# Kernel optimization log

Measured on AMD Instinct MI355X. Metric: run time of the kernel, lower is better.

The kernel has to match this reference:

```python
import jax, jax.numpy as jnp
import numpy as np

B, T = 2, 512
E, NH, HD, V, P, L, KER, BLOCK = 768, 12, 64, 256, 4, 4, 16, 512
SCALE = HD ** -0.5


def _ln(x, g, b, eps=1e-5):
    m = jnp.mean(x, -1, keepdims=True)
    v = jnp.mean((x - m) ** 2, -1, keepdims=True)
    return (x - m) * jax.lax.rsqrt(v + eps) * g + b


def _rope_tables(n):
    inv = 1.0 / (10000.0 ** (jnp.arange(0, HD, 2, dtype=jnp.float32) / HD))
    f = jnp.arange(n, dtype=jnp.float32)[:, None] * inv[None, :]
    return jnp.cos(f), jnp.sin(f)


def _rope(x, cos, sin):
    # rotate over last two dims (positions, HD); split-half RoPE as in source
    h = x.shape[-1] // 2
    x1, x2 = x[..., :h], x[..., h:]
    return jnp.concatenate([x1 * cos - x2 * sin, x1 * sin + x2 * cos], axis=-1)


def _patch_attn(x, qkv_w, S):
    # x: [B,T,E]; sliding-window patch attention, step=1
    Bb, Tt, _ = x.shape
    q, k, v = jnp.split(x @ qkv_w, 3, axis=-1)
    heads = lambda t: t.reshape(Bb, Tt, NH, HD).transpose(0, 2, 1, 3)  # [B,NH,T,HD]
    q, k, v = heads(q), heads(k), heads(v)
    cos, sin = _rope_tables(Tt)
    q = _rope(q, cos, sin)
    k = _rope(k, cos, sin)
    # prefix: full causal attention over first S tokens
    sc = jnp.einsum('bnqh,bnkh->bnqk', q[:, :, :S], k[:, :, :S]) * SCALE
    mask = jnp.tril(jnp.ones((S, S), dtype=bool))
    sc = jnp.where(mask, sc, jnp.float32(-jnp.inf))
    out = jnp.einsum('bnqk,bnkh->bnqh', jax.nn.softmax(sc, axis=-1), v[:, :, :S])
    if Tt > S:
        # query t (t>=S) attends keys [t-S+1, t] (mask_sliding is all-ones for step=1)
        idx = jnp.arange(Tt - S)[:, None] + 1 + jnp.arange(S)[None, :]  # [T-S,S]
        kw = k[:, :, idx]  # [B,NH,T-S,S,HD]
        vw = v[:, :, idx]
        qs = q[:, :, S:]   # [B,NH,T-S,HD]
        sw = jnp.einsum('bnth,bntsh->bnts', qs, kw) * SCALE
        ow = jnp.einsum('bnts,bntsh->bnth', jax.nn.softmax(sw, axis=-1), vw)
        out = jnp.concatenate([out, ow], axis=2)
    return out.transpose(0, 2, 1, 3).reshape(Bb, Tt, NH * HD)


def _sa_block(x, ln0g, ln0b, ln1g, ln1b, qkv_w, proj_w, proj_b, w1, b1, w2, b2):
    # x: [B,T,P,V]; full (unmasked) attention over the P prediction slots
    Bb, Tt, Pp, _ = x.shape
    h = _ln(x, ln0g, ln0b)
    q, k, v = jnp.split(h @ qkv_w, 3, axis=-1)
    heads = lambda t: t.reshape(Bb, Tt, Pp, NH, HD).transpose(0, 1, 3, 2, 4)  # [B,T,NH,P,HD]
    q, k, v = heads(q), heads(k), heads(v)
    cos, sin = _rope_tables(Pp)
    q = _rope(q, cos, sin)
    k = _rope(k, cos, sin)
    sc = jnp.einsum('btnph,btnqh->btnpq', q, k) * SCALE
    o = jnp.einsum('btnpq,btnqh->btnph', jax.nn.softmax(sc, axis=-1), v)
    o = o.transpose(0, 1, 3, 2, 4).reshape(Bb, Tt, Pp, NH * HD)
    x = x + (o @ proj_w + proj_b)
    h2 = _ln(x, ln1g, ln1b)
    ff = jax.nn.gelu(h2 @ w1 + b1, approximate=False) @ w2 + b2
    return x + ff


def _forward(tokens, emb, blk_ln0_g, blk_ln0_b, blk_ln1_g, blk_ln1_b, blk_qkv_w,
             blk_ff_w1, blk_ff_b1, blk_ff_w2, blk_ff_b2, fin_ln_g, fin_ln_b,
             head_w, head_b, sa_ln0_g, sa_ln0_b, sa_ln1_g, sa_ln1_b, sa_qkv_w,
             sa_proj_w, sa_proj_b, sa_ff_w1, sa_ff_b1, sa_ff_w2, sa_ff_b2):
    x0 = emb[tokens]  # [B,T,E]
    x = x0
    for i in range(L):
        S = min(KER * 2 ** i, BLOCK)
        h = _ln(x, blk_ln0_g[i], blk_ln0_b[i])
        x = x + _patch_attn(h, blk_qkv_w[i], S)
        h2 = _ln(x, blk_ln1_g[i], blk_ln1_b[i])
        x = x + (jax.nn.gelu(h2 @ blk_ff_w1[i] + blk_ff_b1[i], approximate=False)
                 @ blk_ff_w2[i] + blk_ff_b2[i])
    x = x0 + x  # Golu: x = token_embedding(x); x = x + blocks(x)
    x = _ln(x, fin_ln_g, fin_ln_b)
    logits = (x @ head_w + head_b).reshape(B, T, P, V)
    logits = _sa_block(logits, sa_ln0_g, sa_ln0_b, sa_ln1_g, sa_ln1_b, sa_qkv_w,
                       sa_proj_w, sa_proj_b, sa_ff_w1, sa_ff_b1, sa_ff_w2, sa_ff_b2)
    return logits[:, :, 0, :]  # [B,T,V] (y is None path)


def setup_inputs() -> dict:
    key = jax.random.key(0)
    ks = jax.random.split(key, 12)
    w = lambda k, sh: jax.random.normal(k, sh, dtype=jnp.float32) * 0.02
    return {
        'tokens': jax.random.randint(ks[0], (B, T), 0, V),
        'emb': w(ks[1], (V, E)),
        'blk_ln0_g': jnp.ones((L, E), jnp.float32),
        'blk_ln0_b': jnp.zeros((L, E), jnp.float32),
        'blk_ln1_g': jnp.ones((L, E), jnp.float32),
        'blk_ln1_b': jnp.zeros((L, E), jnp.float32),
        'blk_qkv_w': w(ks[2], (L, E, 3 * E)),
        'blk_ff_w1': w(ks[3], (L, E, 4 * E)),
        'blk_ff_b1': jnp.zeros((L, 4 * E), jnp.float32),
        'blk_ff_w2': w(ks[4], (L, 4 * E, E)),
        'blk_ff_b2': jnp.zeros((L, E), jnp.float32),
        'fin_ln_g': jnp.ones((E,), jnp.float32),
        'fin_ln_b': jnp.zeros((E,), jnp.float32),
        'head_w': w(ks[5], (E, V * P)),
        'head_b': jnp.zeros((V * P,), jnp.float32),
        'sa_ln0_g': jnp.ones((V,), jnp.float32),
        'sa_ln0_b': jnp.zeros((V,), jnp.float32),
        'sa_ln1_g': jnp.ones((V,), jnp.float32),
        'sa_ln1_b': jnp.zeros((V,), jnp.float32),
        'sa_qkv_w': w(ks[6], (V, 3 * E)),
        'sa_proj_w': w(ks[7], (E, V)),
        'sa_proj_b': jnp.zeros((V,), jnp.float32),
        'sa_ff_w1': w(ks[8], (V, 4 * V)),
        'sa_ff_b1': jnp.zeros((4 * V,), jnp.float32),
        'sa_ff_w2': w(ks[9], (4 * V, V)),
        'sa_ff_b2': jnp.zeros((V,), jnp.float32),
    }


def reference(tokens, emb, blk_ln0_g, blk_ln0_b, blk_ln1_g, blk_ln1_b, blk_qkv_w,
              blk_ff_w1, blk_ff_b1, blk_ff_w2, blk_ff_b2, fin_ln_g, fin_ln_b,
              head_w, head_b, sa_ln0_g, sa_ln0_b, sa_ln1_g, sa_ln1_b, sa_qkv_w,
              sa_proj_w, sa_proj_b, sa_ff_w1, sa_ff_b1, sa_ff_w2, sa_ff_b2):
    return _forward(tokens, emb, blk_ln0_g, blk_ln0_b, blk_ln1_g, blk_ln1_b,
                    blk_qkv_w, blk_ff_w1, blk_ff_b1, blk_ff_w2, blk_ff_b2,
                    fin_ln_g, fin_ln_b, head_w, head_b, sa_ln0_g, sa_ln0_b,
                    sa_ln1_g, sa_ln1_b, sa_qkv_w, sa_proj_w, sa_proj_b,
                    sa_ff_w1, sa_ff_b1, sa_ff_w2, sa_ff_b2)
```

## Files before the change

kernel.cpp:

```cpp
#include <hip/hip_runtime.h>
#include <hip/hip_bf16.h>
#include <cstdint>
#include <cstddef>

#define BB    2
#define TSEQ  512
#define EDIM  768
#define NHEAD 12
#define HDIM  64
#define VDIM  256
#define PDIM  4
#define NROW  (BB*TSEQ)
#define NROW2 (BB*TSEQ*PDIM)

typedef __attribute__((ext_vector_type(8))) short short8;
typedef __attribute__((ext_vector_type(4))) float floatx4;

__device__ __forceinline__ float gelu_f(float v){
    return 0.5f * v * (1.0f + erff(v * 0.70710678118654752f));
}

__device__ __forceinline__ float b2f(short s){
    unsigned u = ((unsigned)(unsigned short)s) << 16;
    float f; __builtin_memcpy(&f, &u, 4); return f;
}

__device__ __forceinline__ void gload16(const void* g, void* l){
    __builtin_amdgcn_global_load_lds((const __attribute__((address_space(1))) void*)g,
                                     (__attribute__((address_space(3))) void*)l, 16, 0, 0);
}

struct WD { const float* in; __hip_bfloat16* out; int K; int N; int ntiles; };

__global__ __launch_bounds__(256) void wconv_multi(WD d0, WD d1, WD d2, WD d3, WD d4)
{
    int id = blockIdx.x;
    WD w = d0;
    if(id >= w.ntiles){ id -= w.ntiles; w = d1;
        if(id >= w.ntiles){ id -= w.ntiles; w = d2;
            if(id >= w.ntiles){ id -= w.ntiles; w = d3;
                if(id >= w.ntiles){ id -= w.ntiles; w = d4; } } } }
    if(!w.in) return;
    const int tx = w.N / 32;
    const int n0 = (id % tx) * 32, k0 = (id / tx) * 32;
    __shared__ float t[32][33];
    const int c = threadIdx.x & 31, r0 = threadIdx.x >> 5;
    #pragma unroll
    for(int r = r0; r < 32; r += 8)
        t[r][c] = w.in[(size_t)(k0 + r) * w.N + n0 + c];
    __syncthreads();
    #pragma unroll
    for(int r = r0; r < 32; r += 8)
        w.out[(size_t)(n0 + r) * w.K + k0 + c] = __float2bfloat16(t[c][r]);
}

template<int ACT, int RESID, int OUTBF16, int ROPESA>
__global__ __launch_bounds__(256) void gemm128(
    const short* __restrict__ A, const short* __restrict__ Bt,
    const float* __restrict__ bias, const float* __restrict__ resid,
    void* __restrict__ Cout, const float* __restrict__ rc, const float* __restrict__ rs,
    int M, int N, int K)
{
    alignas(16) __shared__ short As[128*32];
    alignas(16) __shared__ short Bs[128*32];
    const int tid  = threadIdx.x;
    const int lane = tid & 63;
    const int wave = tid >> 6;
    const int bm = blockIdx.y * 128, bn = blockIdx.x * 128;
    const int wm = (wave >> 1) * 64, wn = (wave & 1) * 64;
    const int quad = lane >> 4, l16 = lane & 15;

    floatx4 acc[4][4];
    #pragma unroll
    for(int i = 0; i < 4; i++)
        #pragma unroll
        for(int j = 0; j < 4; j++)
            acc[i][j] = floatx4{0.f, 0.f, 0.f, 0.f};

    const int r  = tid >> 2;
    const int c8 = (tid & 3) * 8;
    const int ldsoff = (tid & 192) * 16;

    for(int k0 = 0; k0 < K; k0 += 32){
        gload16(A  + (size_t)(bm + r     ) * K + k0 + c8, (char*)As + ldsoff);
        gload16(A  + (size_t)(bm + r + 64) * K + k0 + c8, (char*)As + 4096 + ldsoff);
        gload16(Bt + (size_t)(bn + r     ) * K + k0 + c8, (char*)Bs + ldsoff);
        gload16(Bt + (size_t)(bn + r + 64) * K + k0 + c8, (char*)Bs + 4096 + ldsoff);
        __syncthreads();
        short8 af[4], bfr[4];
        #pragma unroll
        for(int i = 0; i < 4; i++){
            af[i]  = *(const short8*)&As[(wm + i*16 + l16)*32 + quad*8];
            bfr[i] = *(const short8*)&Bs[(wn + i*16 + l16)*32 + quad*8];
        }
        #pragma unroll
        for(int i = 0; i < 4; i++)
            #pragma unroll
            for(int j = 0; j < 4; j++)
                acc[i][j] = __builtin_amdgcn_mfma_f32_16x16x32_bf16(af[i], bfr[j], acc[i][j], 0, 0, 0);
        __syncthreads();
    }

    float* Cf = (float*)Cout;
    __hip_bfloat16* Cb = (__hip_bfloat16*)Cout;

    if(ROPESA){
        const int hb = bn + wn;
        const int region = hb / 768;
        #pragma unroll
        for(int i = 0; i < 4; i++){
            #pragma unroll
            for(int rr = 0; rr < 4; rr++){
                int row = bm + wm + i*16 + quad*4 + rr;
                float a0 = acc[i][0][rr], a1 = acc[i][1][rr];
                float a2 = acc[i][2][rr], a3 = acc[i][3][rr];
                size_t rowb = (size_t)row * N + hb;
                if(region == 2){
                    Cb[rowb + l16]      = __float2bfloat16(a0);
                    Cb[rowb + 16 + l16] = __float2bfloat16(a1);
                    Cb[rowb + 32 + l16] = __float2bfloat16(a2);
                    Cb[rowb + 48 + l16] = __float2bfloat16(a3);
                }else{
                    int p = row & 3;
                    float c0 = rc[p*32 + l16],      s0 = rs[p*32 + l16];
                    float c1 = rc[p*32 + 16 + l16], s1 = rs[p*32 + 16 + l16];
                    Cb[rowb + l16]      = __float2bfloat16(a0*c0 - a2*s0);
                    Cb[rowb + 16 + l16] = __float2bfloat16(a1*c1 - a3*s1);
                    Cb[rowb + 32 + l16] = __float2bfloat16(a0*s0 + a2*c0);
                    Cb[rowb + 48 + l16] = __float2bfloat16(a1*s1 + a3*c1);
                }
            }
        }
        return;
    }

    #pragma unroll
    for(int i = 0; i < 4; i++){
        int row0 = bm + wm + i*16 + quad*4;
        #pragma unroll
        for(int j = 0; j < 4; j++){
            int col = bn + wn + j*16 + l16;
            float bv = bias ? bias[col] : 0.f;
            #pragma unroll
            for(int rr = 0; rr < 4; rr++){
                float v = acc[i][j][rr] + bv;
                if(ACT) v = gelu_f(v);
                if(RESID) v += resid[(size_t)(row0 + rr) * N + col];
                if(OUTBF16) Cb[(size_t)(row0 + rr) * N + col] = __float2bfloat16(v);
                else        Cf[(size_t)(row0 + rr) * N + col] = v;
            }
        }
    }
}

template<int EPI>
__global__ __launch_bounds__(256) void gemm64x128(
    const short* __restrict__ A, const short* __restrict__ Bt,
    const float* __restrict__ bias, __hip_bfloat16* __restrict__ Cout,
    __hip_bfloat16* __restrict__ qrb, __hip_bfloat16* __restrict__ krb,
    __hip_bfloat16* __restrict__ vvb,
    const float* __restrict__ rc, const float* __restrict__ rs,
    int M, int N, int K)
{
    alignas(16) __shared__ short As[64*32];
    alignas(16) __shared__ short Bs[128*32];
    const int tid  = threadIdx.x;
    const int lane = tid & 63;
    const int wave = tid >> 6;
    const int bm = blockIdx.y * 64, bn = blockIdx.x * 128;
    const int wm = (wave >> 1) * 32, wn = (wave & 1) * 64;
    const int quad = lane >> 4, l16 = lane & 15;

    floatx4 acc[2][4];
    #pragma unroll
    for(int i = 0; i < 2; i++)
        #pragma unroll
        for(int j = 0; j < 4; j++)
            acc[i][j] = floatx4{0.f, 0.f, 0.f, 0.f};

    const int r  = tid >> 2;
    const int c8 = (tid & 3) * 8;
    const int ldsoff = (tid & 192) * 16;

    for(int k0 = 0; k0 < K; k0 += 32){
        gload16(A  + (size_t)(bm + r     ) * K + k0 + c8, (char*)As + ldsoff);
        gload16(Bt + (size_t)(bn + r     ) * K + k0 + c8, (char*)Bs + ldsoff);
        gload16(Bt + (size_t)(bn + r + 64) * K + k0 + c8, (char*)Bs + 4096 + ldsoff);
        __syncthreads();
        short8 af[2], bfr[4];
        #pragma unroll
        for(int i = 0; i < 2; i++)
            af[i]  = *(const short8*)&As[(wm + i*16 + l16)*32 + quad*8];
        #pragma unroll
        for(int j = 0; j < 4; j++)
            bfr[j] = *(const short8*)&Bs[(wn + j*16 + l16)*32 + quad*8];
        #pragma unroll
        for(int i = 0; i < 2; i++)
            #pragma unroll
            for(int j = 0; j < 4; j++)
                acc[i][j] = __builtin_amdgcn_mfma_f32_16x16x32_bf16(af[i], bfr[j], acc[i][j], 0, 0, 0);
        __syncthreads();
    }

    if(EPI == 2){
        const int hb = bn + wn;
        const int region = hb / 768;
        const int h = (hb % 768) >> 6;
        #pragma unroll
        for(int i = 0; i < 2; i++){
            #pragma unroll
            for(int rr = 0; rr < 4; rr++){
                int row = bm + wm + i*16 + quad*4 + rr;
                int t = row & (TSEQ-1), b = row >> 9;
                float a0 = acc[i][0][rr], a1 = acc[i][1][rr];
                float a2 = acc[i][2][rr], a3 = acc[i][3][rr];
                size_t dbase = ((size_t)(b*NHEAD + h)*TSEQ + t)*HDIM;
                if(region == 2){
                    vvb[dbase + l16]      = __float2bfloat16(a0);
                    vvb[dbase + 16 + l16] = __float2bfloat16(a1);
                    vvb[dbase + 32 + l16] = __float2bfloat16(a2);
                    vvb[dbase + 48 + l16] = __float2bfloat16(a3);
                }else{
                    float c0 = rc[t*32 + l16],      s0 = rs[t*32 + l16];
                    float c1 = rc[t*32 + 16 + l16], s1 = rs[t*32 + 16 + l16];
                    __hip_bfloat16* dst = (region == 0) ? qrb : krb;
                    dst[dbase + l16]      = __float2bfloat16(a0*c0 - a2*s0);
                    dst[dbase + 16 + l16] = __float2bfloat16(a1*c1 - a3*s1);
                    dst[dbase + 32 + l16] = __float2bfloat16(a0*s0 + a2*c0);
                    dst[dbase + 48 + l16] = __float2bfloat16(a1*s1 + a3*c1);
                }
            }
        }
        return;
    }

    #pragma unroll
    for(int i = 0; i < 2; i++){
        int row0 = bm + wm + i*16 + quad*4;
        #pragma unroll
        for(int j = 0; j < 4; j++){
            int col = bn + wn + j*16 + l16;
            float bv = bias ? bias[col] : 0.f;
            #pragma unroll
            for(int rr = 0; rr < 4; rr++){
                float v = acc[i][j][rr] + bv;
                if(EPI == 1) v = gelu_f(v);
                Cout[(size_t)(row0 + rr) * N + col] = __float2bfloat16(v);
            }
        }
    }
}

template<int ACT, int RESID, int OUTBF16>
__global__ __launch_bounds__(256) void gemm64t(
    const short* __restrict__ A, const short* __restrict__ Bt,
    const float* __restrict__ bias, const float* __restrict__ resid,
    void* __restrict__ Cout, int M, int N, int K)
{
    alignas(16) __shared__ short As[64*32];
    alignas(16) __shared__ short Bs[64*32];
    const int tid  = threadIdx.x;
    const int lane = tid & 63;
    const int wave = tid >> 6;
    const int bm = blockIdx.y * 64, bn = blockIdx.x * 64;
    const int wm = (wave >> 1) * 32, wn = (wave & 1) * 32;
    const int quad = lane >> 4, l16 = lane & 15;

    floatx4 acc[2][2];
    #pragma unroll
    for(int i = 0; i < 2; i++)
        #pragma unroll
        for(int j = 0; j < 2; j++)
            acc[i][j] = floatx4{0.f, 0.f, 0.f, 0.f};

    const int r  = tid >> 2;
    const int c8 = (tid & 3) * 8;
    const int ldsoff = (tid & 192) * 16;

    for(int k0 = 0; k0 < K; k0 += 32){
        gload16(A  + (size_t)(bm + r) * K + k0 + c8, (char*)As + ldsoff);
        gload16(Bt + (size_t)(bn + r) * K + k0 + c8, (char*)Bs + ldsoff);
        __syncthreads();
        short8 af[2], bfr[2];
        #pragma unroll
        for(int i = 0; i < 2; i++){
            af[i]  = *(const short8*)&As[(wm + i*16 + l16)*32 + quad*8];
            bfr[i] = *(const short8*)&Bs[(wn + i*16 + l16)*32 + quad*8];
        }
        #pragma unroll
        for(int i = 0; i < 2; i++)
            #pragma unroll
            for(int j = 0; j < 2; j++)
                acc[i][j] = __builtin_amdgcn_mfma_f32_16x16x32_bf16(af[i], bfr[j], acc[i][j], 0, 0, 0);
        __syncthreads();
    }

    float* Cf = (float*)Cout;
    __hip_bfloat16* Cb = (__hip_bfloat16*)Cout;
    #pragma unroll
    for(int i = 0; i < 2; i++){
        int row0 = bm + wm + i*16 + quad*4;
        #pragma unroll
        for(int j = 0; j < 2; j++){
            int col = bn + wn + j*16 + l16;
            float bv = bias ? bias[col] : 0.f;
            #pragma unroll
            for(int rr = 0; rr < 4; rr++){
                float v = acc[i][j][rr] + bv;
                if(ACT) v = gelu_f(v);
                if(RESID) v += resid[(size_t)(row0 + rr) * N + col];
                if(OUTBF16) Cb[(size_t)(row0 + rr) * N + col] = __float2bfloat16(v);
                else        Cf[(size_t)(row0 + rr) * N + col] = v;
            }
        }
    }
}

__global__ __launch_bounds__(256) void ln_kernel(
    const float* __restrict__ in, const float* __restrict__ in2,
    const float* __restrict__ g, const float* __restrict__ bta,
    __hip_bfloat16* __restrict__ out, int D)
{
    const int row = blockIdx.x;
    const float* xr  = in + (size_t)row * D;
    const float* x2r = in2 ? in2 + (size_t)row * D : nullptr;
    const int tid = threadIdx.x;
    const int nper = D / 256;
    float vals[3];
    float sum = 0.f, sq = 0.f;
    for(int i = 0; i < nper; i++){
        int d = tid + i*256;
        float v = xr[d];
        if(x2r) v += x2r[d];
        vals[i] = v; sum += v; sq += v*v;
    }
    #pragma unroll
    for(int off = 32; off > 0; off >>= 1){
        sum += __shfl_xor(sum, off, 64);
        sq  += __shfl_xor(sq,  off, 64);
    }
    __shared__ float ssum[4], ssq[4];
    __shared__ float smean, srstd;
    int wid = tid >> 6;
    if((tid & 63) == 0){ ssum[wid] = sum; ssq[wid] = sq; }
    __syncthreads();
    if(tid == 0){
        float S = 0.f, Q = 0.f;
        for(int w = 0; w < 4; w++){ S += ssum[w]; Q += ssq[w]; }
        float m = S / D;
        float var = Q / D - m*m;
        smean = m;
        srstd = rsqrtf(fmaxf(var, 0.f) + 1e-5f);
    }
    __syncthreads();
    float m = smean, rs2 = srstd;
    for(int i = 0; i < nper; i++){
        int d = tid + i*256;
        out[(size_t)row*D + d] = __float2bfloat16((vals[i] - m) * rs2 * g[d] + bta[d]);
    }
}

__global__ __launch_bounds__(192) void embed_kernel(
    const int* __restrict__ tokens, const float* __restrict__ emb,
    float* __restrict__ x0, float* __restrict__ x)
{
    const int row = blockIdx.x;
    const int tok = tokens[row];
    const float4* src = (const float4*)(emb + (size_t)tok * EDIM);
    float4* d0 = (float4*)(x0 + (size_t)row * EDIM);
    float4* d1 = (float4*)(x  + (size_t)row * EDIM);
    for(int i = threadIdx.x; i < EDIM/4; i += blockDim.x){
        float4 v = src[i]; d0[i] = v; d1[i] = v;
    }
}

__global__ __launch_bounds__(256) void rope_kernel(float* __restrict__ rc, float* __restrict__ rs)
{
    int i = blockIdx.x * 256 + threadIdx.x;
    int pos = i >> 5, d = i & 31;
    float inv = powf(10000.0f, -(float)(2*d) / 64.0f);
    float f = (float)pos * inv;
    rc[i] = cosf(f);
    rs[i] = sinf(f);
}

template<int S>
__global__ __launch_bounds__(256) void patch_attn2(
    const __hip_bfloat16* __restrict__ qr, const __hip_bfloat16* __restrict__ kr,
    const __hip_bfloat16* __restrict__ vv, float* __restrict__ x)
{
    constexpr int W = S + 3;
    alignas(16) __shared__ short Ks[W*64];
    alignas(16) __shared__ short Vs[W*64];
    __shared__ float qlds[4*64];
    __shared__ float pb[4*128];

    const int t0 = blockIdx.x * 4;
    const int h = blockIdx.y, b = blockIdx.z;
    const int tid = threadIdx.x;
    const int wv = tid >> 6, lane = tid & 63;
    const size_t headbase = ((size_t)(b*NHEAD + h)) * TSEQ;

    const int c = tid & 7;
    for(int r = tid >> 3; r < W; r += 32){
        int g = t0 - S + 1 + r;
        int gc = g < 0 ? 0 : g;
        int sc = (c ^ (r & 7)) * 8;
        *(short8*)&Ks[r*64 + sc] = *(const short8*)((const short*)kr + (headbase + gc)*64 + c*8);
        *(short8*)&Vs[r*64 + sc] = *(const short8*)((const short*)vv + (headbase + gc)*64 + c*8);
    }
    qlds[wv*64 + lane] = __bfloat162float(qr[(headbase + t0 + wv)*64 + lane]);
    __syncthreads();

    const int t = t0 + wv;
    const int r0 = (S >= 64) ? (wv + lane) : ((lane < S) ? (wv + lane) : 0);
    const int r1 = wv + lane + 64;
    float a0 = 0.f, a1 = 0.f;
    #pragma unroll
    for(int ch = 0; ch < 8; ch++){
        float4 qa = *(const float4*)&qlds[wv*64 + ch*8];
        float4 qb = *(const float4*)&qlds[wv*64 + ch*8 + 4];
        short8 k0 = *(const short8*)&Ks[r0*64 + ((ch ^ (r0 & 7))*8)];
        a0 += qa.x*b2f(k0[0]) + qa.y*b2f(k0[1]) + qa.z*b2f(k0[2]) + qa.w*b2f(k0[3])
            + qb.x*b2f(k0[4]) + qb.y*b2f(k0[5]) + qb.z*b2f(k0[6]) + qb.w*b2f(k0[7]);
        if(S == 128){
            short8 k1 = *(const short8*)&Ks[r1*64 + ((ch ^ (r1 & 7))*8)];
            a1 += qa.x*b2f(k1[0]) + qa.y*b2f(k1[1]) + qa.z*b2f(k1[2]) + qa.w*b2f(k1[3])
                + qb.x*b2f(k1[4]) + qb.y*b2f(k1[5]) + qb.z*b2f(k1[6]) + qb.w*b2f(k1[7]);
        }
    }
    const int key0 = t - S + 1 + lane;
    const bool v0 = (lane < S) && (key0 >= 0);
    const bool v1 = (S == 128) && (key0 + 64 >= 0);
    float s0 = v0 ? a0 * 0.125f : -1e30f;
    float s1 = v1 ? a1 * 0.125f : -1e30f;
    float mx = fmaxf(s0, s1);
    #pragma unroll
    for(int off = 32; off > 0; off >>= 1) mx = fmaxf(mx, __shfl_xor(mx, off, 64));
    float p0 = v0 ? expf(s0 - mx) : 0.f;
    float p1 = v1 ? expf(s1 - mx) : 0.f;
    float sm = p0 + p1;
    #pragma unroll
    for(int off = 32; off > 0; off >>= 1) sm += __shfl_xor(sm, off, 64);
    const float inv = 1.f / sm;
    pb[wv*128 + lane] = p0 * inv;
    if(S == 128) pb[wv*128 + lane + 64] = p1 * inv;
    __syncthreads();

    const int d = lane;
    const int coff = d >> 3, dlo = d & 7;
    float o = 0.f;
    #pragma unroll 8
    for(int j = 0; j < S; j++){
        int r = wv + j;
        float p = pb[wv*128 + j];
        o += p * b2f(Vs[r*64 + ((coff ^ (r & 7))*8) + dlo]);
    }
    x[((size_t)(b*TSEQ) + t) * EDIM + h*HDIM + d] += o;
}

__global__ __launch_bounds__(256) void sa_attn(
    const __hip_bfloat16* __restrict__ qkv2, __hip_bfloat16* __restrict__ o)
{
    const int t = blockIdx.x, h = blockIdx.y, b = blockIdx.z;
    const int p = threadIdx.x >> 6, lane = threadIdx.x & 63;
    const int row0 = (b*TSEQ + t) * PDIM;
    const short* base = (const short*)qkv2 + (size_t)row0 * (3*EDIM);
    const int d = lane;
    float q = b2f(base[(size_t)p*(3*EDIM) + h*HDIM + d]);
    float sc[4];
    #pragma unroll
    for(int j = 0; j < 4; j++){
        float kj = b2f(base[(size_t)j*(3*EDIM) + EDIM + h*HDIM + d]);
        float v = q * kj;
        #pragma unroll
        for(int off = 32; off > 0; off >>= 1) v += __shfl_xor(v, off, 64);
        sc[j] = v * 0.125f;
    }
    float m = fmaxf(fmaxf(sc[0], sc[1]), fmaxf(sc[2], sc[3]));
    float e0 = expf(sc[0]-m), e1 = expf(sc[1]-m), e2 = expf(sc[2]-m), e3 = expf(sc[3]-m);
    float idn = 1.f / (e0 + e1 + e2 + e3);
    float ov = (e0 * b2f(base[0*(3*EDIM) + 2*EDIM + h*HDIM + d])
              + e1 * b2f(base[1*(3*EDIM) + 2*EDIM + h*HDIM + d])
              + e2 * b2f(base[2*(3*EDIM) + 2*EDIM + h*HDIM + d])
              + e3 * b2f(base[3*(3*EDIM) + 2*EDIM + h*HDIM + d])) * idn;
    o[(size_t)(row0 + p) * EDIM + h*HDIM + d] = __float2bfloat16(ov);
}

__global__ __launch_bounds__(256) void outcopy(const float* __restrict__ x2, float* __restrict__ out)
{
    int i = blockIdx.x * 256 + threadIdx.x;
    int row = i >> 8, col = i & 255;
    out[i] = x2[(size_t)row * PDIM * VDIM + col];
}

extern "C" void kernel_launch(void* const* d_in, const int* in_sizes, int n_in,
                              void* d_out, int out_size, void* d_ws, size_t ws_size,
                              hipStream_t stream)
{
    const int*   tokens    = (const int*)  d_in[0];
    const float* emb       = (const float*)d_in[1];
    const float* bl0g      = (const float*)d_in[2];
    const float* bl0b      = (const float*)d_in[3];
    const float* bl1g      = (const float*)d_in[4];
    const float* bl1b      = (const float*)d_in[5];
    const float* qkv_w     = (const float*)d_in[6];
    const float* ff_w1     = (const float*)d_in[7];
    const float* ff_b1     = (const float*)d_in[8];
    const float* ff_w2     = (const float*)d_in[9];
    const float* ff_b2     = (const float*)d_in[10];
    const float* fin_g     = (const float*)d_in[11];
    const float* fin_b     = (const float*)d_in[12];
    const float* head_w    = (const float*)d_in[13];
    const float* head_b    = (const float*)d_in[14];
    const float* sa_ln0_g  = (const float*)d_in[15];
    const float* sa_ln0_b  = (const float*)d_in[16];
    const float* sa_ln1_g  = (const float*)d_in[17];
    const float* sa_ln1_b  = (const float*)d_in[18];
    const float* sa_qkv_w  = (const float*)d_in[19];
    const float* sa_proj_w = (const float*)d_in[20];
    const float* sa_proj_b = (const float*)d_in[21];
    const float* sa_ff_w1  = (const float*)d_in[22];
    const float* sa_ff_b1  = (const float*)d_in[23];
    const float* sa_ff_w2  = (const float*)d_in[24];
    const float* sa_ff_b2  = (const float*)d_in[25];
    float* out = (float*)d_out;

    char* base = (char*)d_ws;
    float* logits           = (float*)(base);
    float* ropec            = (float*)(base + 4194304);
    float* ropes            = (float*)(base + 4259840);
    __hip_bfloat16* wqkvT   = (__hip_bfloat16*)(base + 4325376);
    __hip_bfloat16* wff1T   = (__hip_bfloat16*)(base + 7864320);
    __hip_bfloat16* wff2T   = (__hip_bfloat16*)(base + 12582912);
    __hip_bfloat16* wheadT  = (__hip_bfloat16*)(base + 17301504);
    __hip_bfloat16* wsaqkvT = (__hip_bfloat16*)(base + 18874368);
    __hip_bfloat16* wsaprojT= (__hip_bfloat16*)(base + 20054016);
    __hip_bfloat16* wsaff1T = (__hip_bfloat16*)(base + 20447232);
    __hip_bfloat16* wsaff2T = (__hip_bfloat16*)(base + 20971520);
    char* U = base + 21495808;
    float* x0           = (float*)(U);
    float* x            = (float*)(U + 3145728);
    __hip_bfloat16* h   = (__hip_bfloat16*)(U + 6291456);
    __hip_bfloat16* ff1 = (__hip_bfloat16*)(U + 12582912);
    __hip_bfloat16* qrb = (__hip_bfloat16*)(U + 18874368);
    __hip_bfloat16* krb = (__hip_bfloat16*)(U + 20447232);
    __hip_bfloat16* vvb = (__hip_bfloat16*)(U + 22020096);
    __hip_bfloat16* h2    = (__hip_bfloat16*)(U);
    __hip_bfloat16* qkv2  = (__hip_bfloat16*)(U + 2097152);
    __hip_bfloat16* sa_o  = (__hip_bfloat16*)(U + 20971520);
    __hip_bfloat16* sa_f1 = (__hip_bfloat16*)(U + 27262976);

    embed_kernel<<<NROW, 192, 0, stream>>>(tokens, emb, x0, x);
    rope_kernel<<<64, 256, 0, stream>>>(ropec, ropes);
    {
        WD dh  = { head_w,    wheadT,   768,  1024, (1024/32)*( 768/32) };
        WD dq  = { sa_qkv_w,  wsaqkvT,  256,  2304, (2304/32)*( 256/32) };
        WD dp  = { sa_proj_w, wsaprojT, 768,   256, ( 256/32)*( 768/32) };
        WD df1 = { sa_ff_w1,  wsaff1T,  256,  1024, (1024/32)*( 256/32) };
        WD df2 = { sa_ff_w2,  wsaff2T, 1024,   256, ( 256/32)*(1024/32) };
        wconv_multi<<<768+576+192+256+256, 256, 0, stream>>>(dh, dq, dp, df1, df2);
    }

    for(int i = 0; i < 4; i++){
        {
            WD dq  = { qkv_w + (size_t)i*EDIM*3*EDIM, wqkvT, 768, 2304, (2304/32)*(768/32) };
            WD df1 = { ff_w1 + (size_t)i*EDIM*4*EDIM, wff1T, 768, 3072, (3072/32)*(768/32) };
            WD df2 = { ff_w2 + (size_t)i*4*EDIM*EDIM, wff2T, 3072, 768, ( 768/32)*(3072/32)};
            WD dn  = { nullptr, nullptr, 0, 0, 0 };
            wconv_multi<<<1728+2304+2304, 256, 0, stream>>>(dq, df1, df2, dn, dn);
        }
        ln_kernel<<<NROW, 256, 0, stream>>>(x, nullptr, bl0g + i*EDIM, bl0b + i*EDIM, h, EDIM);
        gemm64x128<2><<<dim3(18, 16), 256, 0, stream>>>(
            (const short*)h, (const short*)wqkvT, nullptr, nullptr,
            qrb, krb, vvb, ropec, ropes, NROW, 3*EDIM, EDIM);
        dim3 agrid(TSEQ/4, NHEAD, BB);
        if(i == 0)      patch_attn2<16><<<agrid, 256, 0, stream>>>(qrb, krb, vvb, x);
        else if(i == 1) patch_attn2<32><<<agrid, 256, 0, stream>>>(qrb, krb, vvb, x);
        else if(i == 2) patch_attn2<64><<<agrid, 256, 0, stream>>>(qrb, krb, vvb, x);
        else            patch_attn2<128><<<agrid, 256, 0, stream>>>(qrb, krb, vvb, x);
        ln_kernel<<<NROW, 256, 0, stream>>>(x, nullptr, bl1g + i*EDIM, bl1b + i*EDIM, h, EDIM);
        gemm64x128<1><<<dim3(24, 16), 256, 0, stream>>>(
            (const short*)h, (const short*)wff1T, ff_b1 + (size_t)i*4*EDIM, ff1,
            nullptr, nullptr, nullptr, nullptr, nullptr, NROW, 4*EDIM, EDIM);
        gemm64t<0,1,0><<<dim3(12, 16), 256, 0, stream>>>(
            (const short*)ff1, (const short*)wff2T, ff_b2 + (size_t)i*EDIM, x, x, NROW, EDIM, 4*EDIM);
    }

    ln_kernel<<<NROW, 256, 0, stream>>>(x, x0, fin_g, fin_b, h, EDIM);
    gemm64t<0,0,0><<<dim3(16, 16), 256, 0, stream>>>(
        (const short*)h, (const short*)wheadT, head_b, nullptr, logits, NROW, PDIM*VDIM, EDIM);

    ln_kernel<<<NROW2, 256, 0, stream>>>(logits, nullptr, sa_ln0_g, sa_ln0_b, h2, VDIM);
    gemm128<0,0,1,1><<<dim3(18, 32), 256, 0, stream>>>(
        (const short*)h2, (const short*)wsaqkvT, nullptr, nullptr, qkv2,
        ropec, ropes, NROW2, 3*EDIM, VDIM);
    sa_attn<<<dim3(TSEQ, NHEAD, BB), 256, 0, stream>>>(qkv2, sa_o);
    gemm64t<0,1,0><<<dim3(4, 64), 256, 0, stream>>>(
        (const short*)sa_o, (const short*)wsaprojT, sa_proj_b, logits, logits, NROW2, VDIM, EDIM);
    ln_kernel<<<NROW2, 256, 0, stream>>>(logits, nullptr, sa_ln1_g, sa_ln1_b, h2, VDIM);
    gemm128<1,0,1,0><<<dim3(8, 32), 256, 0, stream>>>(
        (const short*)h2, (const short*)wsaff1T, sa_ff_b1, nullptr, sa_f1,
        nullptr, nullptr, NROW2, 4*VDIM, VDIM);
    gemm64t<0,1,0><<<dim3(4, 64), 256, 0, stream>>>(
        (const short*)sa_f1, (const short*)wsaff2T, sa_ff_b2, logits, logits, NROW2, VDIM, 4*VDIM);

    outcopy<<<(out_size + 255)/256, 256, 0, stream>>>(logits, out);
}
```

Measured before the change: 736.5 us.

## Convert all weights in one launch and fuse output copy into final GEMM

Replaces the per-layer weight transpose/convert launches with a single wconv_all kernel that converts all 17 weight matrices up front into separate per-layer bf16 buffers. It uses 64x64 tiles with float4 loads and short4 stores. The final SA FF2 GEMM now also writes every fourth row (slot 0) directly to the output, which removes the separate outcopy kernel. This cuts launch count and serialization between layers, at the cost of more workspace and a larger struct argument for the kernel.

```diff
diff --git a/kernel.cpp b/kernel.cpp
--- a/kernel.cpp
+++ b/kernel.cpp
@@ -19,39 +19,48 @@
 __device__ __forceinline__ float gelu_f(float v){
     return 0.5f * v * (1.0f + erff(v * 0.70710678118654752f));
 }
-
 __device__ __forceinline__ float b2f(short s){
     unsigned u = ((unsigned)(unsigned short)s) << 16;
     float f; __builtin_memcpy(&f, &u, 4); return f;
 }
-
+__device__ __forceinline__ short f2bs(float v){
+    __hip_bfloat16 h = __float2bfloat16(v);
+    short s; __builtin_memcpy(&s, &h, 2); return s;
+}
 __device__ __forceinline__ void gload16(const void* g, void* l){
     __builtin_amdgcn_global_load_lds((const __attribute__((address_space(1))) void*)g,
                                      (__attribute__((address_space(3))) void*)l, 16, 0, 0);
 }
 
-struct WD { const float* in; __hip_bfloat16* out; int K; int N; int ntiles; };
-
-__global__ __launch_bounds__(256) void wconv_multi(WD d0, WD d1, WD d2, WD d3, WD d4)
+struct WD2 { const float* in; __hip_bfloat16* out; int K; int N; int nt; };
+struct WDs { WD2 d[17]; };
+
+__global__ __launch_bounds__(256) void wconv_all(WDs a)
 {
     int id = blockIdx.x;
-    WD w = d0;
-    if(id >= w.ntiles){ id -= w.ntiles; w = d1;
-        if(id >= w.ntiles){ id -= w.ntiles; w = d2;
-            if(id >= w.ntiles){ id -= w.ntiles; w = d3;
-                if(id >= w.ntiles){ id -= w.ntiles; w = d4; } } } }
-    if(!w.in) return;
-    const int tx = w.N / 32;
-    const int n0 = (id % tx) * 32, k0 = (id / tx) * 32;
-    __shared__ float t[32][33];
-    const int c = threadIdx.x & 31, r0 = threadIdx.x >> 5;
-    #pragma unroll
-    for(int r = r0; r < 32; r += 8)
-        t[r][c] = w.in[(size_t)(k0 + r) * w.N + n0 + c];
+    int i = 0;
+    while(i < 16 && id >= a.d[i].nt){ id -= a.d[i].nt; i++; }
+    WD2 w = a.d[i];
+    const int tx = w.N / 64;
+    const int n0 = (id % tx) * 64, k0 = (id / tx) * 64;
+    __shared__ float t[64][65];
+    const int cg = (threadIdx.x & 15) * 4;
+    const int rr = threadIdx.x >> 4;
+    #pragma unroll
+    for(int it = 0; it < 4; it++){
+        int r = rr + it*16;
+        float4 v = *(const float4*)(w.in + (size_t)(k0 + r) * w.N + n0 + cg);
+        t[r][cg+0] = v.x; t[r][cg+1] = v.y; t[r][cg+2] = v.z; t[r][cg+3] = v.w;
+    }
     __syncthreads();
     #pragma unroll
-    for(int r = r0; r < 32; r += 8)
-        w.out[(size_t)(n0 + r) * w.K + k0 + c] = __float2bfloat16(t[c][r]);
+    for(int it = 0; it < 4; it++){
+        int n = rr + it*16;
+        short4 o;
+        o.x = f2bs(t[cg+0][n]); o.y = f2bs(t[cg+1][n]);
+        o.z = f2bs(t[cg+2][n]); o.w = f2bs(t[cg+3][n]);
+        *(short4*)((short*)w.out + (size_t)(n0 + n) * w.K + k0 + cg) = o;
+    }
 }
 
 template<int ACT, int RESID, int OUTBF16, int ROPESA>
@@ -251,11 +260,11 @@
     }
 }
 
-template<int ACT, int RESID, int OUTBF16>
+template<int RESID, int OUTC>
 __global__ __launch_bounds__(256) void gemm64t(
     const short* __restrict__ A, const short* __restrict__ Bt,
     const float* __restrict__ bias, const float* __restrict__ resid,
-    void* __restrict__ Cout, int M, int N, int K)
+    float* __restrict__ Cf, float* __restrict__ outp, int M, int N, int K)
 {
     alignas(16) __shared__ short As[64*32];
     alignas(16) __shared__ short Bs[64*32];
@@ -295,8 +304,6 @@
         __syncthreads();
     }
 
-    float* Cf = (float*)Cout;
-    __hip_bfloat16* Cb = (__hip_bfloat16*)Cout;
     #pragma unroll
     for(int i = 0; i < 2; i++){
         int row0 = bm + wm + i*16 + quad*4;
@@ -306,11 +313,12 @@
             float bv = bias ? bias[col] : 0.f;
             #pragma unroll
             for(int rr = 0; rr < 4; rr++){
+                int row = row0 + rr;
                 float v = acc[i][j][rr] + bv;
-                if(ACT) v = gelu_f(v);
-                if(RESID) v += resid[(size_t)(row0 + rr) * N + col];
-                if(OUTBF16) Cb[(size_t)(row0 + rr) * N + col] = __float2bfloat16(v);
-                else        Cf[(size_t)(row0 + rr) * N + col] = v;
+                if(RESID) v += resid[(size_t)row * N + col];
+                Cf[(size_t)row * N + col] = v;
+                if(OUTC && (row & 3) == 0)
+                    outp[(size_t)(row >> 2) * N + col] = v;
             }
         }
     }
@@ -485,13 +493,6 @@
               + e2 * b2f(base[2*(3*EDIM) + 2*EDIM + h*HDIM + d])
               + e3 * b2f(base[3*(3*EDIM) + 2*EDIM + h*HDIM + d])) * idn;
     o[(size_t)(row0 + p) * EDIM + h*HDIM + d] = __float2bfloat16(ov);
-}
-
-__global__ __launch_bounds__(256) void outcopy(const float* __restrict__ x2, float* __restrict__ out)
-{
-    int i = blockIdx.x * 256 + threadIdx.x;
-    int row = i >> 8, col = i & 255;
-    out[i] = x2[(size_t)row * PDIM * VDIM + col];
 }
 
 extern "C" void kernel_launch(void* const* d_in, const int* in_sizes, int n_in,
@@ -526,26 +527,28 @@
     const float* sa_ff_b2  = (const float*)d_in[25];
     float* out = (float*)d_out;
 
-    char* base = (char*)d_ws;
-    float* logits           = (float*)(base);
-    float* ropec            = (float*)(base + 4194304);
-    float* ropes            = (float*)(base + 4259840);
-    __hip_bfloat16* wqkvT   = (__hip_bfloat16*)(base + 4325376);
-    __hip_bfloat16* wff1T   = (__hip_bfloat16*)(base + 7864320);
-    __hip_bfloat16* wff2T   = (__hip_bfloat16*)(base + 12582912);
-    __hip_bfloat16* wheadT  = (__hip_bfloat16*)(base + 17301504);
-    __hip_bfloat16* wsaqkvT = (__hip_bfloat16*)(base + 18874368);
-    __hip_bfloat16* wsaprojT= (__hip_bfloat16*)(base + 20054016);
-    __hip_bfloat16* wsaff1T = (__hip_bfloat16*)(base + 20447232);
-    __hip_bfloat16* wsaff2T = (__hip_bfloat16*)(base + 20971520);
-    char* U = base + 21495808;
+    char* p = (char*)d_ws;
+    auto alloc = [&](size_t bytes){ char* q = p; p += (bytes + 255) & ~(size_t)255; return q; };
+
+    float* logits = (float*)alloc((size_t)NROW2*VDIM*4);
+    float* ropec  = (float*)alloc(512*32*4);
+    float* ropes  = (float*)alloc(512*32*4);
+    __hip_bfloat16* wqkvT[4]; for(int i=0;i<4;i++) wqkvT[i] = (__hip_bfloat16*)alloc((size_t)768*2304*2);
+    __hip_bfloat16* wff1T[4]; for(int i=0;i<4;i++) wff1T[i] = (__hip_bfloat16*)alloc((size_t)768*3072*2);
+    __hip_bfloat16* wff2T[4]; for(int i=0;i<4;i++) wff2T[i] = (__hip_bfloat16*)alloc((size_t)3072*768*2);
+    __hip_bfloat16* wheadT   = (__hip_bfloat16*)alloc((size_t)768*1024*2);
+    __hip_bfloat16* wsaqkvT  = (__hip_bfloat16*)alloc((size_t)256*2304*2);
+    __hip_bfloat16* wsaprojT = (__hip_bfloat16*)alloc((size_t)768*256*2);
+    __hip_bfloat16* wsaff1T  = (__hip_bfloat16*)alloc((size_t)256*1024*2);
+    __hip_bfloat16* wsaff2T  = (__hip_bfloat16*)alloc((size_t)1024*256*2);
+    char* U = p;
     float* x0           = (float*)(U);
     float* x            = (float*)(U + 3145728);
     __hip_bfloat16* h   = (__hip_bfloat16*)(U + 6291456);
-    __hip_bfloat16* ff1 = (__hip_bfloat16*)(U + 12582912);
-    __hip_bfloat16* qrb = (__hip_bfloat16*)(U + 18874368);
-    __hip_bfloat16* krb = (__hip_bfloat16*)(U + 20447232);
-    __hip_bfloat16* vvb = (__hip_bfloat16*)(U + 22020096);
+    __hip_bfloat16* ff1 = (__hip_bfloat16*)(U + 7864320);
+    __hip_bfloat16* qrb = (__hip_bfloat16*)(U + 14155776);
+    __hip_bfloat16* krb = (__hip_bfloat16*)(U + 15728640);
+    __hip_bfloat16* vvb = (__hip_bfloat16*)(U + 17301504);
     __hip_bfloat16* h2    = (__hip_bfloat16*)(U);
     __hip_bfloat16* qkv2  = (__hip_bfloat16*)(U + 2097152);
     __hip_bfloat16* sa_o  = (__hip_bfloat16*)(U + 20971520);
@@ -554,25 +557,28 @@
     embed_kernel<<<NROW, 192, 0, stream>>>(tokens, emb, x0, x);
     rope_kernel<<<64, 256, 0, stream>>>(ropec, ropes);
     {
-        WD dh  = { head_w,    wheadT,   768,  1024, (1024/32)*( 768/32) };
-        WD dq  = { sa_qkv_w,  wsaqkvT,  256,  2304, (2304/32)*( 256/32) };
-        WD dp  = { sa_proj_w, wsaprojT, 768,   256, ( 256/32)*( 768/32) };
-        WD df1 = { sa_ff_w1,  wsaff1T,  256,  1024, (1024/32)*( 256/32) };
-        WD df2 = { sa_ff_w2,  wsaff2T, 1024,   256, ( 256/32)*(1024/32) };
-        wconv_multi<<<768+576+192+256+256, 256, 0, stream>>>(dh, dq, dp, df1, df2);
+        WDs wds; int tot = 0, n = 0;
+        auto add = [&](const float* in, __hip_bfloat16* o2, int K, int N){
+            wds.d[n++] = WD2{in, o2, K, N, (N/64)*(K/64)};
+            tot += (N/64)*(K/64);
+        };
+        for(int i=0;i<4;i++){
+            add(qkv_w + (size_t)i*768*2304, wqkvT[i], 768, 2304);
+            add(ff_w1 + (size_t)i*768*3072, wff1T[i], 768, 3072);
+            add(ff_w2 + (size_t)i*3072*768, wff2T[i], 3072, 768);
+        }
+        add(head_w,    wheadT,   768, 1024);
+        add(sa_qkv_w,  wsaqkvT,  256, 2304);
+        add(sa_proj_w, wsaprojT, 768, 256);
+        add(sa_ff_w1,  wsaff1T,  256, 1024);
+        add(sa_ff_w2,  wsaff2T, 1024, 256);
+        wconv_all<<<tot, 256, 0, stream>>>(wds);
     }
 
     for(int i = 0; i < 4; i++){
-        {
-            WD dq  = { qkv_w + (size_t)i*EDIM*3*EDIM, wqkvT, 768, 2304, (2304/32)*(768/32) };
-            WD df1 = { ff_w1 + (size_t)i*EDIM*4*EDIM, wff1T, 768, 3072, (3072/32)*(768/32) };
-            WD df2 = { ff_w2 + (size_t)i*4*EDIM*EDIM, wff2T, 3072, 768, ( 768/32)*(3072/32)};
-            WD dn  = { nullptr, nullptr, 0, 0, 0 };
-            wconv_multi<<<1728+2304+2304, 256, 0, stream>>>(dq, df1, df2, dn, dn);
-        }
         ln_kernel<<<NROW, 256, 0, stream>>>(x, nullptr, bl0g + i*EDIM, bl0b + i*EDIM, h, EDIM);
         gemm64x128<2><<<dim3(18, 16), 256, 0, stream>>>(
-            (const short*)h, (const short*)wqkvT, nullptr, nullptr,
+            (const short*)h, (const short*)wqkvT[i], nullptr, nullptr,
             qrb, krb, vvb, ropec, ropes, NROW, 3*EDIM, EDIM);
         dim3 agrid(TSEQ/4, NHEAD, BB);
         if(i == 0)      patch_attn2<16><<<agrid, 256, 0, stream>>>(qrb, krb, vvb, x);
@@ -581,29 +587,31 @@
         else            patch_attn2<128><<<agrid, 256, 0, stream>>>(qrb, krb, vvb, x);
         ln_kernel<<<NROW, 256, 0, stream>>>(x, nullptr, bl1g + i*EDIM, bl1b + i*EDIM, h, EDIM);
         gemm64x128<1><<<dim3(24, 16), 256, 0, stream>>>(
-            (const short*)h, (const short*)wff1T, ff_b1 + (size_t)i*4*EDIM, ff1,
+            (const short*)h, (const short*)wff1T[i], ff_b1 + (size_t)i*4*EDIM, ff1,
             nullptr, nullptr, nullptr, nullptr, nullptr, NROW, 4*EDIM, EDIM);
-        gemm64t<0,1,0><<<dim3(12, 16), 256, 0, stream>>>(
-            (const short*)ff1, (const short*)wff2T, ff_b2 + (size_t)i*EDIM, x, x, NROW, EDIM, 4*EDIM);
+        gemm64t<1,0><<<dim3(12, 16), 256, 0, stream>>>(
+            (const short*)ff1, (const short*)wff2T[i], ff_b2 + (size_t)i*EDIM, x, x, nullptr,
+            NROW, EDIM, 4*EDIM);
     }
 
     ln_kernel<<<NROW, 256, 0, stream>>>(x, x0, fin_g, fin_b, h, EDIM);
-    gemm64t<0,0,0><<<dim3(16, 16), 256, 0, stream>>>(
-        (const short*)h, (const short*)wheadT, head_b, nullptr, logits, NROW, PDIM*VDIM, EDIM);
+    gemm64t<0,0><<<dim3(16, 16), 256, 0, stream>>>(
+        (const short*)h, (const short*)wheadT, head_b, nullptr, logits, nullptr,
+        NROW, PDIM*VDIM, EDIM);
 
     ln_kernel<<<NROW2, 256, 0, stream>>>(logits, nullptr, sa_ln0_g, sa_ln0_b, h2, VDIM);
     gemm128<0,0,1,1><<<dim3(18, 32), 256, 0, stream>>>(
         (const short*)h2, (const short*)wsaqkvT, nullptr, nullptr, qkv2,
         ropec, ropes, NROW2, 3*EDIM, VDIM);
     sa_attn<<<dim3(TSEQ, NHEAD, BB), 256, 0, stream>>>(qkv2, sa_o);
-    gemm64t<0,1,0><<<dim3(4, 64), 256, 0, stream>>>(
-        (const short*)sa_o, (const short*)wsaprojT, sa_proj_b, logits, logits, NROW2, VDIM, EDIM);
+    gemm64t<1,0><<<dim3(4, 64), 256, 0, stream>>>(
+        (const short*)sa_o, (const short*)wsaprojT, sa_proj_b, logits, logits, nullptr,
+        NROW2, VDIM, EDIM);
     ln_kernel<<<NROW2, 256, 0, stream>>>(logits, nullptr, sa_ln1_g, sa_ln1_b, h2, VDIM);
     gemm128<1,0,1,0><<<dim3(8, 32), 256, 0, stream>>>(
         (const short*)h2, (const short*)wsaff1T, sa_ff_b1, nullptr, sa_f1,
         nullptr, nullptr, NROW2, 4*VDIM, VDIM);
-    gemm64t<0,1,0><<<dim3(4, 64), 256, 0, stream>>>(
-        (const short*)sa_f1, (const short*)wsaff2T, sa_ff_b2, logits, logits, NROW2, VDIM, 4*VDIM);
-
-    outcopy<<<(out_size + 255)/256, 256, 0, stream>>>(logits, out);
-}
+    gemm64t<1,1><<<dim3(4, 64), 256, 0, stream>>>(
+        (const short*)sa_f1, (const short*)wsaff2T, sa_ff_b2, logits, logits, out,
+        NROW2, VDIM, 4*VDIM);
+}
```

New measurement: 704.1 us. -4.4%, faster.
